# Performance work log

Hardware: AMD Instinct MI355X
Metric: run time of the kernel (lower is better)

The kernel has to match this reference:

```python
import jax, jax.numpy as jnp
import numpy as np
import math

D_MODEL = 1024
N_HEADS = 16
HEAD_DIM = D_MODEL // N_HEADS
THETA = 10000.0


def _rope(x, cos, sin):
    # x: [b, h, s, head_dim]; cos/sin: [s, head_dim//2]
    xe = x[..., 0::2]
    xo = x[..., 1::2]
    re = xe * cos - xo * sin
    ro = xe * sin + xo * cos
    # interleave back to even/odd layout
    return jnp.stack([re, ro], axis=-1).reshape(x.shape)


def setup_inputs() -> dict:
    key = jax.random.key(0)
    k1, k2, k3, k4, k5 = jax.random.split(key, 5)
    std = math.sqrt(2.0 / (D_MODEL + D_MODEL))
    x = jax.random.normal(k1, (2, 2048, D_MODEL), dtype=jnp.float32)
    Wq = jax.random.normal(k2, (D_MODEL, D_MODEL), dtype=jnp.float32) * std
    Wk = jax.random.normal(k3, (D_MODEL, D_MODEL), dtype=jnp.float32) * std
    Wv = jax.random.normal(k4, (D_MODEL, D_MODEL), dtype=jnp.float32) * std
    Wo = jax.random.normal(k5, (D_MODEL, D_MODEL), dtype=jnp.float32) * (std / math.sqrt(2))
    return {"x": x, "Wq": Wq, "Wk": Wk, "Wv": Wv, "Wo": Wo}


def reference(x, Wq, Wk, Wv, Wo):
    b, s, d = x.shape
    h, hd = N_HEADS, HEAD_DIM
    # projections: einsum 'batch seq d_in, d_model d_in -> batch seq d_model' == x @ W.T
    def proj(W):
        y = jnp.einsum('bsd,md->bsm', x, W)
        return y.reshape(b, s, h, hd).transpose(0, 2, 1, 3)  # [b, h, s, hd]
    Q, K, V = proj(Wq), proj(Wk), proj(Wv)
    # RoPE with default positions = arange(seq)
    freqs = 1.0 / (THETA ** (jnp.arange(0, hd, 2, dtype=jnp.float32) / hd))
    angles = jnp.arange(s, dtype=jnp.float32)[:, None] * freqs[None, :]  # [s, hd//2]
    cos, sin = jnp.cos(angles), jnp.sin(angles)
    Q = _rope(Q, cos, sin)
    K = _rope(K, cos, sin)
    # naive causal attention
    scores = jnp.einsum('bhqd,bhkd->bhqk', Q, K) / math.sqrt(hd)
    causal = jnp.tril(jnp.ones((s, s), dtype=bool))
    scores = jnp.where(causal, scores, -jnp.inf)
    attn = jax.nn.softmax(scores, axis=-1)
    out = jnp.einsum('bhqk,bhkd->bhqd', attn, V)
    out = out.transpose(0, 2, 1, 3).reshape(b, s, d)
    return jnp.einsum('bsd,md->bsm', out, Wo)
```

## Files before the change

### kernel.cpp

```cpp
#include <hip/hip_runtime.h>
#include <stdint.h>
#include <stddef.h>

typedef __bf16 bf16;
typedef __bf16 bf16x8 __attribute__((ext_vector_type(8)));
typedef __bf16 bf16x4 __attribute__((ext_vector_type(4)));
typedef short short4v __attribute__((ext_vector_type(4)));
typedef float f32x4 __attribute__((ext_vector_type(4)));

#define GAS __attribute__((address_space(1)))
#define LAS __attribute__((address_space(3)))

__device__ __forceinline__ void async_load16(const void* g, void* l) {
  __builtin_amdgcn_global_load_lds((const GAS void*)g, (LAS void*)l, 16, 0, 0);
}

__device__ __forceinline__ f32x4 mfma16(bf16x4 a, bf16x4 b, f32x4 c) {
#if defined(__HIP_DEVICE_COMPILE__)
#if __has_builtin(__builtin_amdgcn_mfma_f32_16x16x16bf16_1k)
  return __builtin_amdgcn_mfma_f32_16x16x16bf16_1k(
      __builtin_bit_cast(short4v, a), __builtin_bit_cast(short4v, b), c, 0, 0, 0);
#else
  f32x4 d;
  asm volatile("v_mfma_f32_16x16x16_bf16 %0, %1, %2, %3"
               : "=v"(d)
               : "v"(a), "v"(b), "v"(c));
  return d;
#endif
#else
  (void)a; (void)b;
  return c;
#endif
}

__global__ __launch_bounds__(256) void cast_all(
    const float* __restrict__ x, const float* __restrict__ Wq,
    const float* __restrict__ Wk, const float* __restrict__ Wv,
    const float* __restrict__ Wo, bf16* __restrict__ Xh,
    bf16* __restrict__ Wqkv, bf16* __restrict__ Woh) {
  int idx = (blockIdx.x * 256 + threadIdx.x) * 4;
  const float* src;
  bf16* dst;
  float scale = 1.0f;
  if (idx < 4194304) {
    src = x + idx; dst = Xh + idx;
  } else if (idx < 7340032) {
    int j = idx - 4194304;
    if (j < 1048576) {
      src = Wq + j; scale = 0.18033688011112042f;
    } else {
      src = ((j < 2097152) ? Wk : Wv) + (j & 1048575);
    }
    dst = Wqkv + j;
  } else {
    int j = idx - 7340032;
    src = Wo + j; dst = Woh + j;
  }
  float4 v = *(const float4*)src;
  bf16x4 o;
  o[0] = (bf16)(v.x * scale); o[1] = (bf16)(v.y * scale);
  o[2] = (bf16)(v.z * scale); o[3] = (bf16)(v.w * scale);
  *(bf16x4*)dst = o;
}

__global__ __launch_bounds__(256) void gemm_qkv(
    const bf16* __restrict__ A, const bf16* __restrict__ B,
    bf16* __restrict__ Qh, bf16* __restrict__ Kh, bf16* __restrict__ Vt,
    int K) {
  __shared__ __align__(16) bf16 As[128 * 32];
  __shared__ __align__(16) bf16 Bs[128 * 32];
  const int tid = threadIdx.x;
  const int wave = tid >> 6, lane = tid & 63;
  const int bm = blockIdx.y * 128, bn = blockIdx.x * 128;
  const int wm = (wave >> 1) * 64, wn = (wave & 1) * 64;
  const int lrow = lane >> 2, lk = (lane & 3) * 8;
  const int fr = lane & 15, fk = (lane >> 4) * 8;

  f32x4 acc[4][4] = {};

  for (int kt = 0; kt < K; kt += 32) {
    __syncthreads();
#pragma unroll
    for (int c = 0; c < 2; ++c) {
      const int chunk = wave * 2 + c;
      const bf16* ga = A + (size_t)(bm + chunk * 16 + lrow) * K + kt + lk;
      async_load16(ga, (void*)(As + chunk * 512));
      const bf16* gb = B + (size_t)(bn + chunk * 16 + lrow) * K + kt + lk;
      async_load16(gb, (void*)(Bs + chunk * 512));
    }
    __syncthreads();

    bf16x8 af[4], bfr[4];
#pragma unroll
    for (int i = 0; i < 4; ++i)
      af[i] = *(const bf16x8*)&As[(wm + i * 16 + fr) * 32 + fk];
#pragma unroll
    for (int j = 0; j < 4; ++j)
      bfr[j] = *(const bf16x8*)&Bs[(wn + j * 16 + fr) * 32 + fk];
#pragma unroll
    for (int i = 0; i < 4; ++i)
#pragma unroll
      for (int j = 0; j < 4; ++j)
        acc[i][j] =
            __builtin_amdgcn_mfma_f32_16x16x32_bf16(af[i], bfr[j], acc[i][j], 0, 0, 0);
  }

  const int r0 = (lane >> 4) * 4, cc = lane & 15;
  const bool oddl = cc & 1;
#pragma unroll
  for (int i = 0; i < 4; ++i) {
    const int row0 = bm + wm + i * 16 + r0;
    const int b = row0 >> 11, s0 = row0 & 2047;
#pragma unroll
    for (int j = 0; j < 4; ++j) {
      const int col = bn + wn + j * 16 + cc;
      if (col < 2048) {
        const int hcol = col & 1023;
        const int h = hcol >> 6, d = hcol & 63;
        const int ip = d >> 1;
        const float freq = __expf((float)ip * -0.2878231366242557f);
        const bool isK = col >= 1024;
        bf16* dst = (isK ? Kh : Qh) + ((size_t)(b * 16 + h) * 2048) * 64;
#pragma unroll
        for (int r = 0; r < 4; ++r) {
          float own = acc[i][j][r];
          float oth = __shfl_xor(own, 1, 64);
          float sn, cs;
          __sincosf((float)(s0 + r) * freq, &sn, &cs);
          float res = oddl ? (oth * sn + own * cs) : (own * cs - oth * sn);
          const int dd = isK ? (d ^ (((s0 + r) & 7) << 3)) : d;
          dst[(size_t)(s0 + r) * 64 + dd] = (bf16)res;
        }
      } else {
        const int v = col - 2048, h = v >> 6, d = v & 63;
        bf16x4 o;
#pragma unroll
        for (int r = 0; r < 4; ++r) o[r] = (bf16)acc[i][j][r];
        const int s2 = (s0 & ~63) | ((s0 ^ ((d & 7) << 3)) & 63);
        *(bf16x4*)&Vt[(((size_t)b * 16 + h) * 64 + d) * 2048 + s2] = o;
      }
    }
  }
}

template <typename OutT, int BM, int BN>
__global__ __launch_bounds__(256) void gemm_bt(
    const bf16* __restrict__ A, const bf16* __restrict__ B,
    OutT* __restrict__ C, int M, int N, int K) {
  constexpr int ACH = BM / 16, NCH = (BM + BN) / 16, PW = NCH / 4;
  constexpr int FM = BM / 32, FN = BN / 32;
  __shared__ __align__(16) bf16 As[BM * 32];
  __shared__ __align__(16) bf16 Bs[BN * 32];
  const int tid = threadIdx.x;
  const int wave = tid >> 6, lane = tid & 63;
  const int bm = blockIdx.y * BM, bn = blockIdx.x * BN;
  const int wm = (wave >> 1) * (BM / 2), wn = (wave & 1) * (BN / 2);
  const int lrow = lane >> 2, lk = (lane & 3) * 8;
  const int fr = lane & 15, fk = (lane >> 4) * 8;

  f32x4 acc[FM][FN] = {};

  for (int kt = 0; kt < K; kt += 32) {
    __syncthreads();
#pragma unroll
    for (int c = 0; c < PW; ++c) {
      const int chunk = wave * PW + c;
      if (chunk < ACH) {
        const bf16* ga = A + (size_t)(bm + chunk * 16 + lrow) * K + kt + lk;
        async_load16(ga, (void*)(As + chunk * 512));
      } else {
        const int bc = chunk - ACH;
        const bf16* gb = B + (size_t)(bn + bc * 16 + lrow) * K + kt + lk;
        async_load16(gb, (void*)(Bs + bc * 512));
      }
    }
    __syncthreads();

    bf16x8 af[FM], bfr[FN];
#pragma unroll
    for (int i = 0; i < FM; ++i)
      af[i] = *(const bf16x8*)&As[(wm + i * 16 + fr) * 32 + fk];
#pragma unroll
    for (int j = 0; j < FN; ++j)
      bfr[j] = *(const bf16x8*)&Bs[(wn + j * 16 + fr) * 32 + fk];
#pragma unroll
    for (int i = 0; i < FM; ++i)
#pragma unroll
      for (int j = 0; j < FN; ++j)
        acc[i][j] =
            __builtin_amdgcn_mfma_f32_16x16x32_bf16(af[i], bfr[j], acc[i][j], 0, 0, 0);
  }

  const int r0 = (lane >> 4) * 4, cc = lane & 15;
#pragma unroll
  for (int i = 0; i < FM; ++i)
#pragma unroll
    for (int j = 0; j < FN; ++j)
#pragma unroll
      for (int r = 0; r < 4; ++r)
        C[(size_t)(bm + wm + i * 16 + r0 + r) * N + (bn + wn + j * 16 + cc)] =
            (OutT)acc[i][j][r];
}

__global__ __launch_bounds__(256, 2) void attn(const bf16* __restrict__ Qh,
                                               const bf16* __restrict__ Kh,
                                               const bf16* __restrict__ Vt,
                                               bf16* __restrict__ Oh) {
  __shared__ __align__(16) bf16 Ks[2][64 * 64];
  __shared__ __align__(16) bf16 Vs[2][64 * 64];
  const int f = blockIdx.x;
  const int j = 15 - (f >> 5);
  const int bh = f & 31;
  const int tid = threadIdx.x, w = tid >> 6, lane = tid & 63;
  const int nlo = lane & 15, g = lane >> 4;
  const int q0 = j * 128, qw0 = q0 + w * 32;
  const bf16* __restrict__ Qp = Qh + (size_t)bh * 131072;
  const bf16* __restrict__ Kp = Kh + (size_t)bh * 131072;
  const bf16* __restrict__ Vp = Vt + (size_t)bh * 131072;
  const int n = 2 * (j + 1);

  bf16x8 aq[2][2];
#pragma unroll
  for (int qb = 0; qb < 2; ++qb)
#pragma unroll
    for (int ks = 0; ks < 2; ++ks)
      aq[qb][ks] =
          *(const bf16x8*)&Qp[(size_t)(qw0 + qb * 16 + nlo) * 64 + ks * 32 + g * 8];

  f32x4 oacc[2][4] = {};
  float lsum[2] = {0.f, 0.f};
  const int sw = (nlo & 7) << 3;

  const int srow = w * 16 + (lane >> 3);
  const int soff = (lane & 7) * 8;

  auto stage = [&](int buf, int kbase) {
    async_load16(Kp + (size_t)(kbase + srow) * 64 + soff,
                 (void*)(Ks[buf] + w * 1024));
    async_load16(Kp + (size_t)(kbase + srow + 8) * 64 + soff,
                 (void*)(Ks[buf] + w * 1024 + 512));
    async_load16(Vp + (size_t)srow * 2048 + kbase + soff,
                 (void*)(Vs[buf] + w * 1024));
    async_load16(Vp + (size_t)(srow + 8) * 2048 + kbase + soff,
                 (void*)(Vs[buf] + w * 1024 + 512));
  };

  stage(0, 0);
  __syncthreads();

  for (int i = 0; i < n; ++i) {
    const int buf = i & 1, kbase = i * 64;
    if (i + 1 < n) stage(buf ^ 1, (i + 1) * 64);

    if (kbase <= qw0 + 31) {
      const bf16* __restrict__ Kw = Ks[buf];
      const bf16* __restrict__ Vw = Vs[buf];

      bf16x8 pk[4][2];
#pragma unroll
      for (int ni = 0; ni < 4; ++ni)
#pragma unroll
        for (int ks = 0; ks < 2; ++ks)
          pk[ni][ks] = *(const bf16x8*)&Kw[(ni * 16 + nlo) * 64 +
                                           ((ks * 32 + g * 8) ^ sw)];

      const bool dg = (kbase + 63 > qw0);
      bf16x4 p[2][4];
#pragma unroll
      for (int qb = 0; qb < 2; ++qb) {
        f32x4 st[4] = {};
#pragma unroll
        for (int ks = 0; ks < 2; ++ks)
#pragma unroll
          for (int ni = 0; ni < 4; ++ni)
            st[ni] = __builtin_amdgcn_mfma_f32_16x16x32_bf16(pk[ni][ks], aq[qb][ks],
                                                             st[ni], 0, 0, 0);
        const int qg = qw0 + qb * 16 + nlo;
        if (!dg) {
#pragma unroll
          for (int ni = 0; ni < 4; ++ni)
#pragma unroll
            for (int r = 0; r < 4; ++r) {
              float e = __builtin_amdgcn_exp2f(st[ni][r]);
              lsum[qb] += e;
              p[qb][ni][r] = (bf16)e;
            }
        } else {
#pragma unroll
          for (int ni = 0; ni < 4; ++ni) {
            const int kg0 = kbase + ni * 16 + g * 4;
#pragma unroll
            for (int r = 0; r < 4; ++r) {
              float e = __builtin_amdgcn_exp2f(st[ni][r]);
              e = (kg0 + r <= qg) ? e : 0.0f;
              lsum[qb] += e;
              p[qb][ni][r] = (bf16)e;
            }
          }
        }
      }

      bf16x4 av[4][4];
#pragma unroll
      for (int ni = 0; ni < 4; ++ni)
#pragma unroll
        for (int mi = 0; mi < 4; ++mi)
          av[ni][mi] = *(const bf16x4*)&Vw[(mi * 16 + nlo) * 64 +
                                           ((ni * 16 + g * 4) ^ sw)];
#pragma unroll
      for (int ni = 0; ni < 4; ++ni)
#pragma unroll
        for (int mi = 0; mi < 4; ++mi)
#pragma unroll
          for (int qb = 0; qb < 2; ++qb)
            oacc[qb][mi] = mfma16(av[ni][mi], p[qb][ni], oacc[qb][mi]);
    }

    __syncthreads();
  }

#pragma unroll
  for (int qb = 0; qb < 2; ++qb) {
    lsum[qb] += __shfl_xor(lsum[qb], 16, 64);
    lsum[qb] += __shfl_xor(lsum[qb], 32, 64);
  }

  const int bb = bh >> 4, hd = bh & 15;
#pragma unroll
  for (int qb = 0; qb < 2; ++qb) {
    const float inv = 1.0f / lsum[qb];
    const int q = qw0 + qb * 16 + nlo;
#pragma unroll
    for (int mi = 0; mi < 4; ++mi) {
      bf16x4 o;
#pragma unroll
      for (int r = 0; r < 4; ++r) o[r] = (bf16)(oacc[qb][mi][r] * inv);
      *(bf16x4*)&Oh[((size_t)bb * 2048 + q) * 1024 + hd * 64 + mi * 16 + g * 4] = o;
    }
  }
}

extern "C" void kernel_launch(void* const* d_in, const int* in_sizes, int n_in,
                              void* d_out, int out_size, void* d_ws, size_t ws_size,
                              hipStream_t stream) {
  (void)in_sizes; (void)n_in; (void)out_size; (void)ws_size;
  const float* x = (const float*)d_in[0];
  const float* Wq = (const float*)d_in[1];
  const float* Wk = (const float*)d_in[2];
  const float* Wv = (const float*)d_in[3];
  const float* Wo = (const float*)d_in[4];
  float* out = (float*)d_out;
  char* ws = (char*)d_ws;

  bf16* Xh   = (bf16*)(ws);
  bf16* Wqkv = (bf16*)(ws + 8388608);
  bf16* Woh  = (bf16*)(ws + 14680064);
  bf16* Qh   = (bf16*)(ws + 16777216);
  bf16* Kh   = (bf16*)(ws + 25165824);
  bf16* Vt   = (bf16*)(ws + 33554432);
  bf16* Oh   = (bf16*)(ws + 41943040);

  cast_all<<<8192, 256, 0, stream>>>(x, Wq, Wk, Wv, Wo, Xh, Wqkv, Woh);
  gemm_qkv<<<dim3(24, 32), 256, 0, stream>>>(Xh, Wqkv, Qh, Kh, Vt, 1024);
  attn<<<512, 256, 0, stream>>>(Qh, Kh, Vt, Oh);
  gemm_bt<float, 128, 128><<<dim3(8, 32), 256, 0, stream>>>(Oh, Woh, out, 4096, 1024, 1024);
}
```

Measured before the change: 194.8 us.

## Software-pipeline attention loop with triple buffering and reordered block schedule

Moves from double to triple-buffered K/V LDS tiles, staging two tiles ahead. The loop is restructured so each iteration runs QK^T for the next tile alongside PV for the current one, with s_setprio raised around the MFMA section. This lets exp work overlap matrix work. The block-to-(head, q-tile) mapping is also changed to pair long and short causal tiles across batches. The cost is more LDS per block, which may limit occupancy, and more register pressure from the extra live state.

After: 190.0 us. -2.5%, faster.

```diff
diff --git a/kernel.cpp b/kernel.cpp
--- a/kernel.cpp
+++ b/kernel.cpp
@@ -206,11 +206,12 @@
                                                const bf16* __restrict__ Kh,
                                                const bf16* __restrict__ Vt,
                                                bf16* __restrict__ Oh) {
-  __shared__ __align__(16) bf16 Ks[2][64 * 64];
-  __shared__ __align__(16) bf16 Vs[2][64 * 64];
+  __shared__ __align__(16) bf16 Ks[3][64 * 64];
+  __shared__ __align__(16) bf16 Vs[3][64 * 64];
   const int f = blockIdx.x;
-  const int j = 15 - (f >> 5);
-  const int bh = f & 31;
+  int j, bh;
+  if (f < 256) { bh = f >> 4;              j = 15 - (f & 15); }
+  else         { bh = 16 + ((f - 256) >> 4); j = f & 15; }
   const int tid = threadIdx.x, w = tid >> 6, lane = tid & 63;
   const int nlo = lane & 15, g = lane >> 4;
   const int q0 = j * 128, qw0 = q0 + w * 32;
@@ -218,6 +219,7 @@
   const bf16* __restrict__ Kp = Kh + (size_t)bh * 131072;
   const bf16* __restrict__ Vp = Vt + (size_t)bh * 131072;
   const int n = 2 * (j + 1);
+  const int nw = 2 * j + (w >> 1) + 1;
 
   bf16x8 aq[2][2];
 #pragma unroll
@@ -234,89 +236,120 @@
   const int srow = w * 16 + (lane >> 3);
   const int soff = (lane & 7) * 8;
 
-  auto stage = [&](int buf, int kbase) {
+  auto stage = [&](int slot, int kbase) {
     async_load16(Kp + (size_t)(kbase + srow) * 64 + soff,
-                 (void*)(Ks[buf] + w * 1024));
+                 (void*)(Ks[slot] + w * 1024));
     async_load16(Kp + (size_t)(kbase + srow + 8) * 64 + soff,
-                 (void*)(Ks[buf] + w * 1024 + 512));
+                 (void*)(Ks[slot] + w * 1024 + 512));
     async_load16(Vp + (size_t)srow * 2048 + kbase + soff,
-                 (void*)(Vs[buf] + w * 1024));
+                 (void*)(Vs[slot] + w * 1024));
     async_load16(Vp + (size_t)(srow + 8) * 2048 + kbase + soff,
-                 (void*)(Vs[buf] + w * 1024 + 512));
-  };
-
-  stage(0, 0);
-  __syncthreads();
-
-  for (int i = 0; i < n; ++i) {
-    const int buf = i & 1, kbase = i * 64;
-    if (i + 1 < n) stage(buf ^ 1, (i + 1) * 64);
-
-    if (kbase <= qw0 + 31) {
-      const bf16* __restrict__ Kw = Ks[buf];
-      const bf16* __restrict__ Vw = Vs[buf];
-
-      bf16x8 pk[4][2];
-#pragma unroll
-      for (int ni = 0; ni < 4; ++ni)
-#pragma unroll
-        for (int ks = 0; ks < 2; ++ks)
-          pk[ni][ks] = *(const bf16x8*)&Kw[(ni * 16 + nlo) * 64 +
-                                           ((ks * 32 + g * 8) ^ sw)];
-
-      const bool dg = (kbase + 63 > qw0);
-      bf16x4 p[2][4];
-#pragma unroll
-      for (int qb = 0; qb < 2; ++qb) {
-        f32x4 st[4] = {};
-#pragma unroll
-        for (int ks = 0; ks < 2; ++ks)
-#pragma unroll
-          for (int ni = 0; ni < 4; ++ni)
-            st[ni] = __builtin_amdgcn_mfma_f32_16x16x32_bf16(pk[ni][ks], aq[qb][ks],
-                                                             st[ni], 0, 0, 0);
-        const int qg = qw0 + qb * 16 + nlo;
-        if (!dg) {
-#pragma unroll
-          for (int ni = 0; ni < 4; ++ni)
-#pragma unroll
-            for (int r = 0; r < 4; ++r) {
-              float e = __builtin_amdgcn_exp2f(st[ni][r]);
-              lsum[qb] += e;
-              p[qb][ni][r] = (bf16)e;
-            }
-        } else {
-#pragma unroll
-          for (int ni = 0; ni < 4; ++ni) {
-            const int kg0 = kbase + ni * 16 + g * 4;
-#pragma unroll
-            for (int r = 0; r < 4; ++r) {
-              float e = __builtin_amdgcn_exp2f(st[ni][r]);
-              e = (kg0 + r <= qg) ? e : 0.0f;
-              lsum[qb] += e;
-              p[qb][ni][r] = (bf16)e;
-            }
+                 (void*)(Vs[slot] + w * 1024 + 512));
+  };
+
+  bf16x8 pk[4][2];
+  auto rdK = [&](int slot) {
+    const bf16* __restrict__ Kw = Ks[slot];
+#pragma unroll
+    for (int ni = 0; ni < 4; ++ni)
+#pragma unroll
+      for (int ks = 0; ks < 2; ++ks)
+        pk[ni][ks] =
+            *(const bf16x8*)&Kw[(ni * 16 + nlo) * 64 + ((ks * 32 + g * 8) ^ sw)];
+  };
+
+  bf16x4 av[4][4];
+  auto rdV = [&](int slot) {
+    const bf16* __restrict__ Vw = Vs[slot];
+#pragma unroll
+    for (int ni = 0; ni < 4; ++ni)
+#pragma unroll
+      for (int mi = 0; mi < 4; ++mi)
+        av[ni][mi] =
+            *(const bf16x4*)&Vw[(mi * 16 + nlo) * 64 + ((ni * 16 + g * 4) ^ sw)];
+  };
+
+  f32x4 st[2][4];
+  auto qk = [&]() {
+#pragma unroll
+    for (int qb = 0; qb < 2; ++qb) {
+#pragma unroll
+      for (int ni = 0; ni < 4; ++ni) st[qb][ni] = f32x4{0.f, 0.f, 0.f, 0.f};
+#pragma unroll
+      for (int ks = 0; ks < 2; ++ks)
+#pragma unroll
+        for (int ni = 0; ni < 4; ++ni)
+          st[qb][ni] = __builtin_amdgcn_mfma_f32_16x16x32_bf16(
+              pk[ni][ks], aq[qb][ks], st[qb][ni], 0, 0, 0);
+    }
+  };
+
+  bf16x4 p[2][4];
+  auto expv = [&](int i) {
+    const int kbase = i * 64;
+    const bool dg = (i == nw - 1);
+#pragma unroll
+    for (int qb = 0; qb < 2; ++qb) {
+      const int qg = qw0 + qb * 16 + nlo;
+      if (!dg) {
+#pragma unroll
+        for (int ni = 0; ni < 4; ++ni)
+#pragma unroll
+          for (int r = 0; r < 4; ++r) {
+            float e = __builtin_amdgcn_exp2f(st[qb][ni][r]);
+            lsum[qb] += e;
+            p[qb][ni][r] = (bf16)e;
+          }
+      } else {
+#pragma unroll
+        for (int ni = 0; ni < 4; ++ni) {
+          const int kg0 = kbase + ni * 16 + g * 4;
+#pragma unroll
+          for (int r = 0; r < 4; ++r) {
+            float e = __builtin_amdgcn_exp2f(st[qb][ni][r]);
+            e = (kg0 + r <= qg) ? e : 0.0f;
+            lsum[qb] += e;
+            p[qb][ni][r] = (bf16)e;
           }
         }
       }
-
-      bf16x4 av[4][4];
-#pragma unroll
-      for (int ni = 0; ni < 4; ++ni)
-#pragma unroll
-        for (int mi = 0; mi < 4; ++mi)
-          av[ni][mi] = *(const bf16x4*)&Vw[(mi * 16 + nlo) * 64 +
-                                           ((ni * 16 + g * 4) ^ sw)];
-#pragma unroll
-      for (int ni = 0; ni < 4; ++ni)
-#pragma unroll
-        for (int mi = 0; mi < 4; ++mi)
-#pragma unroll
-          for (int qb = 0; qb < 2; ++qb)
-            oacc[qb][mi] = mfma16(av[ni][mi], p[qb][ni], oacc[qb][mi]);
-    }
-
+    }
+  };
+
+  auto pv = [&]() {
+#pragma unroll
+    for (int ni = 0; ni < 4; ++ni)
+#pragma unroll
+      for (int mi = 0; mi < 4; ++mi)
+#pragma unroll
+        for (int qb = 0; qb < 2; ++qb)
+          oacc[qb][mi] = mfma16(av[ni][mi], p[qb][ni], oacc[qb][mi]);
+  };
+
+  stage(0, 0);
+  stage(1, 64);
+  __syncthreads();
+  rdK(0);
+  qk();
+  expv(0);
+
+  for (int i = 0; i < n - 1; ++i) {
+    const int i1 = i + 1;
+    if (i + 2 < n) stage((i + 2) % 3, (i + 2) * 64);
+    const bool doQK = (i1 < nw);
+    if (doQK) rdK(i1 % 3);
+    rdV(i % 3);
+    __builtin_amdgcn_s_setprio(1);
+    if (doQK) qk();
+    pv();
+    __builtin_amdgcn_s_setprio(0);
+    if (doQK) expv(i1);
     __syncthreads();
+  }
+
+  if (nw == n) {
+    rdV((n - 1) % 3);
+    pv();
   }
 
 #pragma unroll
```
